# Optimization experiments

Measured on AMD Instinct MI355X. Metric: run time of the kernel, lower is better.

The kernel has to match this reference:

```python
import jax, jax.numpy as jnp
import numpy as np

HEADS = 4
DIM_HEAD = 128

def setup_inputs() -> dict:
    key = jax.random.key(0)
    k1, k2, k3, k4 = jax.random.split(key, 4)
    scale = DIM_HEAD ** -0.5
    return {
        "fmap": jax.random.normal(k1, (16, 512, 32, 32), dtype=jnp.float32),
        "w_qkv": jax.random.normal(k2, (1536, 512), dtype=jnp.float32) * 0.02,
        "height": jax.random.normal(k3, (32, DIM_HEAD), dtype=jnp.float32) * scale,
        "width": jax.random.normal(k4, (32, DIM_HEAD), dtype=jnp.float32) * scale,
    }

def reference(fmap, w_qkv, height, width):
    b, c, h, w = fmap.shape
    scale = DIM_HEAD ** -0.5
    # 1x1 conv == channel GEMM: (b, 3*heads*dim_head, h, w)
    qkv = jnp.einsum('bchw,oc->bohw', fmap, w_qkv)
    # split into q,k,v and reshape to (b, heads, seq, dim_head)
    qkv = qkv.reshape(b, 3, HEADS, DIM_HEAD, h * w)
    q, k, v = (jnp.transpose(qkv[:, i], (0, 1, 3, 2)) for i in range(3))
    # content logits
    sim = jnp.einsum('bhid,bhjd->bhij', q, k) * scale
    # absolute positional bias: emb[(x,y)] = height[x] + width[y]
    emb = (height[:, None, :] + width[None, :, :]).reshape(h * w, DIM_HEAD)
    sim = sim + jnp.einsum('bhid,jd->bhij', q, emb) * scale
    attn = jax.nn.softmax(sim, axis=-1)
    out = jnp.einsum('bhij,bhjd->bhid', attn, v)  # (b, heads, seq, d)
    out = jnp.transpose(out, (0, 1, 3, 2)).reshape(b, HEADS * DIM_HEAD, h, w)
    return out
```

## Files before the change

kernel.cpp:

```cpp
#include <hip/hip_runtime.h>
#include <math.h>

#define HEADS 4
#define DIMH  128
#define NB    16
#define CIN   512
#define SEQ   1024
#define OTOT  1536
#define KQ    (CIN / 8)

typedef __attribute__((ext_vector_type(8)))  short bf16x8;
typedef __attribute__((ext_vector_type(4)))  short bf16x4;
typedef __attribute__((ext_vector_type(4)))  float f32x4;
typedef __attribute__((ext_vector_type(16))) float f32x16;

#define MFMA16(a,b,c) __builtin_amdgcn_mfma_f32_16x16x32_bf16(a,b,c,0,0,0)
#define MFMA32(a,b,c) __builtin_amdgcn_mfma_f32_32x32x16_bf16(a,b,c,0,0,0)

__device__ __forceinline__ short f2bf(float f) {
    unsigned u = __builtin_bit_cast(unsigned, f);
    u = (u + 0x7FFFu + ((u >> 16) & 1u)) >> 16;
    return (short)u;
}
__device__ __forceinline__ unsigned pk2(float lo, float hi) {
    return __builtin_amdgcn_perm(__builtin_bit_cast(unsigned, hi),
                                 __builtin_bit_cast(unsigned, lo), 0x07060302u);
}
union PF8 { unsigned u[4]; bf16x8 v; };

__global__ __launch_bounds__(256) void convert_fmap(const float* __restrict__ F,
                                                    short* __restrict__ FT2) {
    const int s  = blockIdx.x * 256 + threadIdx.x;
    const int kq = blockIdx.y, b = blockIdx.z;
    const float* src = F + ((size_t)b * CIN + kq * 8) * SEQ + s;
    float v[8];
    #pragma unroll
    for (int i = 0; i < 8; ++i) v[i] = src[(size_t)i * SEQ];
    bf16x8 pk = { f2bf(v[0]), f2bf(v[1]), f2bf(v[2]), f2bf(v[3]),
                  f2bf(v[4]), f2bf(v[5]), f2bf(v[6]), f2bf(v[7]) };
    *(bf16x8*)&FT2[(((size_t)b * KQ + kq) * SEQ + s) * 8] = pk;
}

__global__ __launch_bounds__(256) void convert_w(const float* __restrict__ W,
                                                 short* __restrict__ Wb2) {
    const int o  = blockIdx.x * 256 + threadIdx.x;
    const int kq = blockIdx.y;
    float4 v0 = *(const float4*)&W[(size_t)o * CIN + kq * 8];
    float4 v1 = *(const float4*)&W[(size_t)o * CIN + kq * 8 + 4];
    bf16x8 pk = { f2bf(v0.x), f2bf(v0.y), f2bf(v0.z), f2bf(v0.w),
                  f2bf(v1.x), f2bf(v1.y), f2bf(v1.z), f2bf(v1.w) };
    *(bf16x8*)&Wb2[((size_t)kq * OTOT + o) * 8] = pk;
}

__global__ __launch_bounds__(256, 3) void qkv_gemm(
    const short* __restrict__ Wb2, const short* __restrict__ FT2,
    const float* __restrict__ height, const float* __restrict__ width,
    short* __restrict__ Qo, short* __restrict__ Kfo, short* __restrict__ Vfo)
{
    const int b = blockIdx.z, o0 = blockIdx.y * 128, s0 = blockIdx.x * 128;
    const int t = threadIdx.x, l = t & 63, w = t >> 6;
    const int quad = l >> 4, ln = l & 15;
    const int wrow = (w >> 1) * 64, wcol = (w & 1) * 64;

    const short* Ap = Wb2 + (((size_t)quad * OTOT) + (o0 + wrow + ln)) * 8;
    const short* Bp = FT2 + ((((size_t)b * KQ + quad) * SEQ) + (s0 + wcol + ln)) * 8;

    f32x4 acc[4][4] = {};
    bf16x8 a0[4], b0[4], a1[4], b1[4];

#define GLOADF(ks, af, bfr) { \
    const short* ga = Ap + (size_t)(ks) * 4 * OTOT * 8; \
    const short* gb = Bp + (size_t)(ks) * 4 * SEQ * 8; \
    _Pragma("unroll") for (int i = 0; i < 4; ++i) af[i]  = *(const bf16x8*)(ga + (size_t)i * 16 * 8); \
    _Pragma("unroll") for (int j = 0; j < 4; ++j) bfr[j] = *(const bf16x8*)(gb + (size_t)j * 16 * 8); }
#define COMP(af, bfr) { \
    _Pragma("unroll") for (int i = 0; i < 4; ++i) \
        _Pragma("unroll") for (int j = 0; j < 4; ++j) \
            acc[i][j] = MFMA16(af[i], bfr[j], acc[i][j]); }

    GLOADF(0, a0, b0);
    GLOADF(1, a1, b1);
    for (int ks = 0; ks < 16; ks += 2) {
        COMP(a0, b0);
        if (ks + 2 < 16) GLOADF(ks + 2, a0, b0);
        COMP(a1, b1);
        if (ks + 3 < 16) GLOADF(ks + 3, a1, b1);
    }

    const int sec = o0 >> 9;
    const int h   = (o0 >> 7) & 3;
    const size_t bh = (size_t)b * HEADS + h;

    if (sec == 0) {
        const float qs = 0.08838834764831845f * 1.4426950408889634f;
        #pragma unroll
        for (int ti = 0; ti < 4; ++ti) {
            int d = wrow + ti * 16 + quad * 4;
            #pragma unroll
            for (int tj = 0; tj < 4; ++tj) {
                int s = s0 + wcol + tj * 16 + ln;
                f32x4 a = acc[ti][tj];
                bf16x4 pk4 = { f2bf(a[0]*qs), f2bf(a[1]*qs), f2bf(a[2]*qs), f2bf(a[3]*qs) };
                *(bf16x4*)&Qo[(bh * SEQ + s) * DIMH + d] = pk4;
            }
        }
    } else if (sec == 1) {
        #pragma unroll
        for (int ti = 0; ti < 4; ++ti) {
            int d = wrow + ti * 16 + quad * 4;
            #pragma unroll
            for (int tj = 0; tj < 4; ++tj) {
                int s = s0 + wcol + tj * 16 + ln;
                float4 hv = *(const float4*)&height[(size_t)(s >> 5) * DIMH + d];
                float4 wv = *(const float4*)&width[(size_t)(s & 31) * DIMH + d];
                f32x4 a = acc[ti][tj];
                bf16x4 pk4 = { f2bf(a[0] + hv.x + wv.x), f2bf(a[1] + hv.y + wv.y),
                               f2bf(a[2] + hv.z + wv.z), f2bf(a[3] + hv.w + wv.w) };
                *(bf16x4*)&Kfo[(((size_t)bh * 16 + (d >> 3)) * SEQ + s) * 8 + (d & 7)] = pk4;
            }
        }
    } else {
        const int slot = ((ln >> 2) & 1) * 8 + (ln & 3) + ((ln >> 3) << 2);
        #pragma unroll
        for (int ti = 0; ti < 4; ++ti) {
            int d = wrow + ti * 16 + quad * 4;
            #pragma unroll
            for (int tj = 0; tj < 4; ++tj) {
                int s = s0 + wcol + tj * 16 + ln;
                size_t vb = (((size_t)bh * 64 + (s >> 4)) * DIMH) * 16 + slot;
                f32x4 a = acc[ti][tj];
                #pragma unroll
                for (int r = 0; r < 4; ++r)
                    Vfo[vb + (size_t)(d + r) * 16] = f2bf(a[r]);
            }
        }
    }
}

#define BQ 128
#define BJ 64
#define KSTR 136

__global__ __launch_bounds__(256, 2) void attn(
    const short* __restrict__ Q, const short* __restrict__ Kf,
    const short* __restrict__ Vf, float* __restrict__ out)
{
    __shared__ short Ks[2 * BJ * KSTR];

    const int t = threadIdx.x, l = t & 63, w = t >> 6;
    const int h = l >> 5, c31 = l & 31;

    const int L = blockIdx.x;
    const int x = L & 7, inner = L >> 3;
    const int bh = x * 8 + (inner >> 3);
    const int q0 = (inner & 7) * BQ;
    const size_t obase = (size_t)bh * DIMH * SEQ;

    bf16x8 qf[8];
    {
        const short* Qp = Q + ((size_t)bh * SEQ + (q0 + w * 32 + c31)) * DIMH + h * 8;
        #pragma unroll
        for (int kc = 0; kc < 8; ++kc)
            qf[kc] = *(const bf16x8*)(Qp + kc * 16);
    }

    PF8 ones;
    ones.u[0] = ones.u[1] = ones.u[2] = ones.u[3] = 0x3F803F80u;

    const short* Kg = Kf + (size_t)bh * 16 * SEQ * 8;
    const short* Vlane = Vf + (size_t)bh * 64 * (DIMH * 16) + (c31 * 16 + h * 8);

    f32x16 O[4] = {};
    f32x16 Lacc = {};

    {
        int4 kreg[4];
        #pragma unroll
        for (int p = 0; p < 4; ++p)
            kreg[p] = *(const int4*)(Kg + ((size_t)(p * 4 + w) * SEQ + l) * 8);
        #pragma unroll
        for (int p = 0; p < 4; ++p)
            *(int4*)&Ks[l * KSTR + (p * 4 + w) * 8] = kreg[p];
    }
    __syncthreads();

    for (int ti = 0; ti < 16; ++ti) {
        const int cur = (ti & 1) * (BJ * KSTR);
        const int nxt = (BJ * KSTR) - cur;
        int4 kreg[4];
        if (ti < 15) {
            const int j0n = (ti + 1) * BJ;
            #pragma unroll
            for (int p = 0; p < 4; ++p)
                kreg[p] = *(const int4*)(Kg + ((size_t)(p * 4 + w) * SEQ + j0n + l) * 8);
        }

        f32x16 S0 = {}, S1 = {};
        #pragma unroll
        for (int kc = 0; kc < 8; ++kc) {
            bf16x8 k0 = *(const bf16x8*)&Ks[cur + c31 * KSTR + kc * 16 + h * 8];
            bf16x8 k1 = *(const bf16x8*)&Ks[cur + (32 + c31) * KSTR + kc * 16 + h * 8];
            S0 = MFMA32(k0, qf[kc], S0);
            S1 = MFMA32(k1, qf[kc], S1);
        }

        const int jgb = ti * 4;
        #pragma unroll
        for (int half = 0; half < 2; ++half) {
            const f32x16& S = half ? S1 : S0;
            #pragma unroll
            for (int kk = 0; kk < 2; ++kk) {
                PF8 pf;
                #pragma unroll
                for (int m = 0; m < 4; ++m) {
                    float a = __builtin_amdgcn_exp2f(S[kk * 8 + 2 * m]);
                    float b = __builtin_amdgcn_exp2f(S[kk * 8 + 2 * m + 1]);
                    pf.u[m] = pk2(a, b);
                }
                Lacc = MFMA32(ones.v, pf.v, Lacc);
                const short* vp = Vlane + (size_t)(jgb + half * 2 + kk) * (DIMH * 16);
                #pragma unroll
                for (int dc = 0; dc < 4; ++dc) {
                    bf16x8 vf = *(const bf16x8*)(vp + dc * 32 * 16);
                    O[dc] = MFMA32(vf, pf.v, O[dc]);
                }
            }
        }

        if (ti < 15) {
            #pragma unroll
            for (int p = 0; p < 4; ++p)
                *(int4*)&Ks[nxt + l * KSTR + (p * 4 + w) * 8] = kreg[p];
        }
        __syncthreads();
    }

    float linv = 1.0f / Lacc[0];
    #pragma unroll
    for (int dc = 0; dc < 4; ++dc)
        #pragma unroll
        for (int r = 0; r < 16; ++r) {
            int d = dc * 32 + (r & 3) + 8 * (r >> 2) + 4 * h;
            out[obase + (size_t)d * SEQ + q0 + w * 32 + c31] = O[dc][r] * linv;
        }
}

extern "C" void kernel_launch(void* const* d_in, const int* in_sizes, int n_in,
                              void* d_out, int out_size, void* d_ws, size_t ws_size,
                              hipStream_t stream) {
    const float* fmap   = (const float*)d_in[0];
    const float* w_qkv  = (const float*)d_in[1];
    const float* height = (const float*)d_in[2];
    const float* width  = (const float*)d_in[3];
    float* outp = (float*)d_out;

    const size_t n_ft  = (size_t)NB * SEQ * CIN;
    const size_t n_w   = (size_t)OTOT * CIN;
    const size_t n_qkv = (size_t)NB * HEADS * SEQ * DIMH;

    short* FT2 = (short*)d_ws;
    short* Wb2 = FT2 + n_ft;
    short* Qb  = Wb2 + n_w;
    short* Kfb = Qb + n_qkv;
    short* Vfb = Kfb + n_qkv;

    convert_fmap<<<dim3(SEQ / 256, KQ, NB), 256, 0, stream>>>(fmap, FT2);
    convert_w<<<dim3(OTOT / 256, KQ), 256, 0, stream>>>(w_qkv, Wb2);
    qkv_gemm<<<dim3(SEQ / 128, OTOT / 128, NB), 256, 0, stream>>>(
        Wb2, FT2, height, width, Qb, Kfb, Vfb);
    attn<<<dim3(NB * HEADS * (SEQ / BQ)), 256, 0, stream>>>(Qb, Kfb, Vfb, outp);
}
```

Before: 196.8 us.

## Remap GEMM grid to 1D, prefetch V into registers, replace row-sum MFMA

The QKV GEMM launch becomes a 1D grid with a block-index remapping meant to spread or group blocks across XCDs for better L2 reuse. In the attention kernel, all V fragments for a tile are loaded into registers at the start of each iteration so the loads overlap the QK MFMAs. The softmax denominator is now accumulated with scalar adds plus a cross-lane shuffle instead of an extra MFMA against a ones vector. This raises register pressure (64 extra VGPRs for V) and sums in fp32 rather than over bf16-rounded probabilities, which slightly changes numerics.

```diff
diff --git a/kernel.cpp b/kernel.cpp
--- a/kernel.cpp
+++ b/kernel.cpp
@@ -57,7 +57,13 @@
     const float* __restrict__ height, const float* __restrict__ width,
     short* __restrict__ Qo, short* __restrict__ Kfo, short* __restrict__ Vfo)
 {
-    const int b = blockIdx.z, o0 = blockIdx.y * 128, s0 = blockIdx.x * 128;
+    const int L  = blockIdx.x;
+    const int x8 = L & 7, m = L >> 3;
+    const int g  = x8 + 8 * (m / 12);
+    const int oy = m % 12;
+    const int b  = g >> 3, sx = g & 7;
+    const int o0 = oy * 128, s0 = sx * 128;
+
     const int t = threadIdx.x, l = t & 63, w = t >> 6;
     const int quad = l >> 4, ln = l & 15;
     const int wrow = (w >> 1) * 64, wcol = (w & 1) * 64;
@@ -164,14 +170,11 @@
             qf[kc] = *(const bf16x8*)(Qp + kc * 16);
     }
 
-    PF8 ones;
-    ones.u[0] = ones.u[1] = ones.u[2] = ones.u[3] = 0x3F803F80u;
-
     const short* Kg = Kf + (size_t)bh * 16 * SEQ * 8;
     const short* Vlane = Vf + (size_t)bh * 64 * (DIMH * 16) + (c31 * 16 + h * 8);
 
     f32x16 O[4] = {};
-    f32x16 Lacc = {};
+    float psum = 0.f;
 
     {
         int4 kreg[4];
@@ -187,6 +190,16 @@
     for (int ti = 0; ti < 16; ++ti) {
         const int cur = (ti & 1) * (BJ * KSTR);
         const int nxt = (BJ * KSTR) - cur;
+
+        bf16x8 vreg[4][4];
+        {
+            const short* vp0 = Vlane + (size_t)(ti * 4) * (DIMH * 16);
+            #pragma unroll
+            for (int gi = 0; gi < 4; ++gi)
+                #pragma unroll
+                for (int dc = 0; dc < 4; ++dc)
+                    vreg[gi][dc] = *(const bf16x8*)(vp0 + (size_t)gi * (DIMH * 16) + dc * 32 * 16);
+        }
         int4 kreg[4];
         if (ti < 15) {
             const int j0n = (ti + 1) * BJ;
@@ -204,7 +217,6 @@
             S1 = MFMA32(k1, qf[kc], S1);
         }
 
-        const int jgb = ti * 4;
         #pragma unroll
         for (int half = 0; half < 2; ++half) {
             const f32x16& S = half ? S1 : S0;
@@ -215,15 +227,13 @@
                 for (int m = 0; m < 4; ++m) {
                     float a = __builtin_amdgcn_exp2f(S[kk * 8 + 2 * m]);
                     float b = __builtin_amdgcn_exp2f(S[kk * 8 + 2 * m + 1]);
+                    psum += a + b;
                     pf.u[m] = pk2(a, b);
                 }
-                Lacc = MFMA32(ones.v, pf.v, Lacc);
-                const short* vp = Vlane + (size_t)(jgb + half * 2 + kk) * (DIMH * 16);
-                #pragma unroll
-                for (int dc = 0; dc < 4; ++dc) {
-                    bf16x8 vf = *(const bf16x8*)(vp + dc * 32 * 16);
-                    O[dc] = MFMA32(vf, pf.v, O[dc]);
-                }
+                const int gi = half * 2 + kk;
+                #pragma unroll
+                for (int dc = 0; dc < 4; ++dc)
+                    O[dc] = MFMA32(vreg[gi][dc], pf.v, O[dc]);
             }
         }
 
@@ -235,7 +245,9 @@
         __syncthreads();
     }
 
-    float linv = 1.0f / Lacc[0];
+    psum += __shfl_xor(psum, 32);
+    float linv = 1.0f / psum;
+
     #pragma unroll
     for (int dc = 0; dc < 4; ++dc)
         #pragma unroll
@@ -266,7 +278,7 @@
 
     convert_fmap<<<dim3(SEQ / 256, KQ, NB), 256, 0, stream>>>(fmap, FT2);
     convert_w<<<dim3(OTOT / 256, KQ), 256, 0, stream>>>(w_qkv, Wb2);
-    qkv_gemm<<<dim3(SEQ / 128, OTOT / 128, NB), 256, 0, stream>>>(
+    qkv_gemm<<<dim3(8 * 12 * NB), 256, 0, stream>>>(
         Wb2, FT2, height, width, Qb, Kfb, Vfb);
     attn<<<dim3(NB * HEADS * (SEQ / BQ)), 256, 0, stream>>>(Qb, Kfb, Vfb, outp);
 }
```

Result: faster. 176.5 us (-10.3%).
